# Kernel optimization log

Measured on AMD Instinct MI355X. Metric: run time of the kernel, lower is better.

The kernel has to match this reference:

```python
import jax, jax.numpy as jnp
import numpy as np

TEMP = 0.5
EPS = 1e-12  # matches torch F.normalize default eps


def _l2_normalize(x):
    n = jnp.sqrt(jnp.sum(x * x, axis=1, keepdims=True))
    return x / jnp.maximum(n, EPS)


def setup_inputs() -> dict:
    key = jax.random.key(0)
    k1, k2 = jax.random.split(key)
    B, D = 4096, 256
    return {
        "x_i": jax.random.normal(k1, (B, D), dtype=jnp.float32),
        "x_j": jax.random.normal(k2, (B, D), dtype=jnp.float32),
    }


def reference(x_i, x_j):
    B = x_i.shape[0]
    z = jnp.concatenate([_l2_normalize(x_i), _l2_normalize(x_j)], axis=0)  # [2B, D]
    # cosine similarity of normalized vectors == plain matmul
    sim = z @ z.T  # [2B, 2B]
    pos = jnp.concatenate([jnp.diagonal(sim, B), jnp.diagonal(sim, -B)], axis=0)  # [2B]
    neg_mask = 1.0 - jnp.eye(2 * B, dtype=sim.dtype)
    denom = jnp.sum(neg_mask * jnp.exp(sim / TEMP), axis=1)  # [2B]
    # -log(exp(pos/T) / denom) = -pos/T + log(denom)
    loss = jnp.sum(-(pos / TEMP) + jnp.log(denom)) / (2 * B)
    return loss
```

## Files before the change

### kernel.cpp

```cpp
#include <hip/hip_runtime.h>
#include <hip/hip_bf16.h>

#define B_ROWS 4096
#define NROWS  8192
#define D      256
#define TT     264
#define NBLK2  512
#define MAXT   9

typedef __attribute__((ext_vector_type(8))) short bf16x8;
typedef __attribute__((ext_vector_type(4))) float floatx4;

__global__ __launch_bounds__(256) void norm_pos_kernel(
    const float* __restrict__ xi, const float* __restrict__ xj,
    short* __restrict__ z, float* __restrict__ pos,
    float* __restrict__ selfdot, float* __restrict__ rowsum,
    float* __restrict__ out, unsigned int* __restrict__ counter) {
    int gt = blockIdx.x * 256 + threadIdx.x;
    if (gt < NROWS) rowsum[gt] = 0.f;
    if (gt == 0) { out[0] = 0.f; counter[0] = 0u; }

    int p    = blockIdx.x * 4 + (threadIdx.x >> 6);
    int lane = threadIdx.x & 63;
    float4 v1 = ((const float4*)(xi + (size_t)p * D))[lane];
    float4 v2 = ((const float4*)(xj + (size_t)p * D))[lane];
    float ss1 = v1.x * v1.x + v1.y * v1.y + v1.z * v1.z + v1.w * v1.w;
    float ss2 = v2.x * v2.x + v2.y * v2.y + v2.z * v2.z + v2.w * v2.w;
#pragma unroll
    for (int off = 32; off > 0; off >>= 1) {
        ss1 += __shfl_xor(ss1, off);
        ss2 += __shfl_xor(ss2, off);
    }
    float sc1 = 1.0f / fmaxf(sqrtf(ss1), 1e-12f);
    float sc2 = 1.0f / fmaxf(sqrtf(ss2), 1e-12f);

    union { __hip_bfloat16 h[4]; short4 s4; } u1, u2;
    u1.h[0] = __float2bfloat16(v1.x * sc1); u1.h[1] = __float2bfloat16(v1.y * sc1);
    u1.h[2] = __float2bfloat16(v1.z * sc1); u1.h[3] = __float2bfloat16(v1.w * sc1);
    u2.h[0] = __float2bfloat16(v2.x * sc2); u2.h[1] = __float2bfloat16(v2.y * sc2);
    u2.h[2] = __float2bfloat16(v2.z * sc2); u2.h[3] = __float2bfloat16(v2.w * sc2);
    ((short4*)(z + (size_t)p * D))[lane]            = u1.s4;
    ((short4*)(z + (size_t)(p + B_ROWS) * D))[lane] = u2.s4;

    float sd1 = 0.f, sd2 = 0.f, dp = 0.f;
#pragma unroll
    for (int j = 0; j < 4; j++) {
        float a = __bfloat162float(u1.h[j]);
        float b = __bfloat162float(u2.h[j]);
        sd1 += a * a; sd2 += b * b; dp += a * b;
    }
#pragma unroll
    for (int off = 32; off > 0; off >>= 1) {
        sd1 += __shfl_xor(sd1, off);
        sd2 += __shfl_xor(sd2, off);
        dp  += __shfl_xor(dp,  off);
    }
    if (lane == 0) {
        pos[p] = dp; pos[p + B_ROWS] = dp;
        selfdot[p] = sd1; selfdot[p + B_ROWS] = sd2;
    }
}

__global__ __launch_bounds__(256, 2) void sim_rowsum_kernel(
    const short* __restrict__ z, float* __restrict__ rowsum,
    const float* __restrict__ pos, const float* __restrict__ selfdot,
    unsigned int* __restrict__ counter, float* __restrict__ out) {
    __shared__ __align__(16) short Bbuf[2][8192];
    __shared__ float mirror_lds[MAXT][32];
    __shared__ unsigned int done_s;
    __shared__ float sdata[4];

    const int tid  = threadIdx.x;
    const int lane = tid & 63;
    const int w    = tid >> 6;
    const int lm   = lane & 15;
    const int lg   = lane >> 4;
    const int fxor = lm & 7;

    const int s   = blockIdx.x >> 5;
    const int q   = blockIdx.x & 31;
    const int L0  = 256 - 8 * s;
    const int cb  = (q * TT) >> 5;
    const int ce  = ((q + 1) * TT) >> 5;

    bf16x8 a[8][4];
    floatx4 acc[4][2];
    float rsacc[4][4];

#pragma unroll
    for (int mi = 0; mi < 4; mi++)
#pragma unroll
        for (int r = 0; r < 4; r++) rsacc[mi][r] = 0.f;

    auto decode = [&](int c, int& panel, int& colbase, bool& mirror) {
        int cloc;
        if (c < L0) { panel = s;      cloc = c; }
        else        { panel = 31 - s; cloc = c - L0; }
        colbase = panel * 256 + cloc * 32;
        mirror  = (cloc >= 8);
    };

    auto decodeCol = [&](int c) {
        int cloc, panel;
        if (c < L0) { panel = s;      cloc = c; }
        else        { panel = 31 - s; cloc = c - L0; }
        return panel * 256 + cloc * 32;
    };

    auto loadA = [&](int panel) {
#pragma unroll
        for (int kk = 0; kk < 8; kk++)
#pragma unroll
            for (int mi = 0; mi < 4; mi++)
                a[kk][mi] = *(const bf16x8*)(
                    z + (size_t)(panel * 256 + w * 64 + mi * 16 + lm) * D +
                    kk * 32 + lg * 8);
    };

    auto flushRs = [&](int panel) {
#pragma unroll
        for (int mi = 0; mi < 4; mi++)
#pragma unroll
            for (int r = 0; r < 4; r++) {
                float v = rsacc[mi][r];
                v += __shfl_xor(v, 1); v += __shfl_xor(v, 2);
                v += __shfl_xor(v, 4); v += __shfl_xor(v, 8);
                if (lm == 0)
                    atomicAdd(&rowsum[panel * 256 + w * 64 + mi * 16 + lg * 4 + r], v);
                rsacc[mi][r] = 0.f;
            }
    };

    auto stage = [&](int buf, int colbase) {
#pragma unroll
        for (int j = 0; j < 4; j++) {
            int col = w * 8 + j * 2 + (lane >> 5);
            int c16 = (lane & 31) ^ (col & 7);
            const short* src = z + (size_t)(colbase + col) * D + c16 * 8;
            __builtin_amdgcn_global_load_lds(
                (const __attribute__((address_space(1))) unsigned int*)src,
                (__attribute__((address_space(3))) unsigned int*)
                    &Bbuf[buf][(w * 4 + j) * 512],
                16, 0, 0);
        }
    };

    for (int e = tid; e < MAXT * 32; e += 256)
        ((float*)mirror_lds)[e] = 0.f;

    int panel, colbase; bool mirror;
    decode(cb, panel, colbase, mirror);
    int curpanel = panel;
    stage(0, colbase);
    loadA(panel);
    __syncthreads();

    for (int c = cb; c < ce; c++) {
        const int buf = (c - cb) & 1;
        decode(c, panel, colbase, mirror);

        if (c + 1 < ce)
            stage(buf ^ 1, decodeCol(c + 1));

        if (panel != curpanel) {
            flushRs(curpanel);
            loadA(panel);
            curpanel = panel;
        }

#pragma unroll
        for (int mi = 0; mi < 4; mi++)
#pragma unroll
            for (int ni = 0; ni < 2; ni++)
                acc[mi][ni] = (floatx4){0.f, 0.f, 0.f, 0.f};

#pragma unroll
        for (int kk = 0; kk < 8; kk++) {
            bf16x8 b0 = *(const bf16x8*)(
                &Bbuf[buf][((lm) * 32 + ((kk * 4 + lg) ^ fxor)) * 8]);
            bf16x8 b1 = *(const bf16x8*)(
                &Bbuf[buf][((16 + lm) * 32 + ((kk * 4 + lg) ^ fxor)) * 8]);
#pragma unroll
            for (int mi = 0; mi < 4; mi++)
                acc[mi][0] = __builtin_amdgcn_mfma_f32_16x16x32_bf16(
                    a[kk][mi], b0, acc[mi][0], 0, 0, 0);
#pragma unroll
            for (int mi = 0; mi < 4; mi++)
                acc[mi][1] = __builtin_amdgcn_mfma_f32_16x16x32_bf16(
                    a[kk][mi], b1, acc[mi][1], 0, 0, 0);
        }

        float cs0 = 0.f, cs1 = 0.f;
#pragma unroll
        for (int mi = 0; mi < 4; mi++)
#pragma unroll
            for (int r = 0; r < 4; r++) {
                float e0 = __expf(2.0f * acc[mi][0][r]);
                float e1 = __expf(2.0f * acc[mi][1][r]);
                rsacc[mi][r] += e0 + e1;
                cs0 += e0; cs1 += e1;
            }
        if (mirror) {
            cs0 += __shfl_xor(cs0, 16); cs0 += __shfl_xor(cs0, 32);
            cs1 += __shfl_xor(cs1, 16); cs1 += __shfl_xor(cs1, 32);
            if (lane < 16) {
                atomicAdd(&mirror_lds[c - cb][lane],      cs0);
                atomicAdd(&mirror_lds[c - cb][16 + lane], cs1);
            }
        }

        __syncthreads();
    }
    flushRs(curpanel);

    __syncthreads();
    {
        const int nt = ce - cb;
        for (int e = tid; e < nt * 32; e += 256) {
            int t = e >> 5, col = e & 31;
            int p2, cbase2; bool m2;
            decode(cb + t, p2, cbase2, m2);
            if (m2) atomicAdd(&rowsum[cbase2 + col], mirror_lds[t][col]);
        }
    }

    __syncthreads();
    if (tid == 0) {
        __threadfence();
        done_s = atomicAdd(counter, 1u);
    }
    __syncthreads();
    if (done_s == (unsigned int)(NBLK2 - 1)) {
        __threadfence();
        float acc_l = 0.f;
#pragma unroll 4
        for (int r = tid; r < NROWS; r += 256) {
            float rsv = __hip_atomic_load(&rowsum[r], __ATOMIC_RELAXED,
                                          __HIP_MEMORY_SCOPE_AGENT);
            float denom = rsv - __expf(2.0f * selfdot[r]);
            acc_l += -2.0f * pos[r] + logf(denom);
        }
#pragma unroll
        for (int off = 32; off > 0; off >>= 1) acc_l += __shfl_xor(acc_l, off);
        if (lane == 0) sdata[w] = acc_l;
        __syncthreads();
        if (tid == 0)
            out[0] = (sdata[0] + sdata[1] + sdata[2] + sdata[3]) / (float)NROWS;
    }
}

extern "C" void kernel_launch(void* const* d_in, const int* in_sizes, int n_in,
                              void* d_out, int out_size, void* d_ws, size_t ws_size,
                              hipStream_t stream) {
    const float* xi = (const float*)d_in[0];
    const float* xj = (const float*)d_in[1];
    float* out      = (float*)d_out;

    char* ws        = (char*)d_ws;
    short* z        = (short*)ws;
    float* rowsum   = (float*)(ws + (size_t)NROWS * D * 2);
    float* pos      = rowsum + NROWS;
    float* selfdot  = pos + NROWS;
    unsigned int* counter = (unsigned int*)(selfdot + NROWS);

    norm_pos_kernel<<<B_ROWS / 4, 256, 0, stream>>>(xi, xj, z, pos, selfdot,
                                                    rowsum, out, counter);
    sim_rowsum_kernel<<<NBLK2, 256, 0, stream>>>(z, rowsum, pos, selfdot,
                                                 counter, out);
}
```

Before: 103.7 us.

## Widen column tiles to 64 and push mirror sums straight to global atomics

Doubles the per-iteration column tile from 32 to 64 columns, so each wave computes a 64x64 block with 16 accumulators. This halves the number of tiles, block barriers and staging rounds per block, and each A-fragment load is reused across four B fragments. The LDS mirror-sum buffer and its final flush loop are removed. Mirror column sums now go directly to global rowsum with atomics from inside the loop. The change doubles the LDS staging buffer, raises register pressure from the larger accumulator array, and puts global atomics on the critical path of each iteration.

```diff
diff --git a/kernel.cpp b/kernel.cpp
--- a/kernel.cpp
+++ b/kernel.cpp
@@ -4,9 +4,8 @@
 #define B_ROWS 4096
 #define NROWS  8192
 #define D      256
-#define TT     264
+#define TT     132
 #define NBLK2  512
-#define MAXT   9
 
 typedef __attribute__((ext_vector_type(8))) short bf16x8;
 typedef __attribute__((ext_vector_type(4))) float floatx4;
@@ -65,8 +64,7 @@
     const short* __restrict__ z, float* __restrict__ rowsum,
     const float* __restrict__ pos, const float* __restrict__ selfdot,
     unsigned int* __restrict__ counter, float* __restrict__ out) {
-    __shared__ __align__(16) short Bbuf[2][8192];
-    __shared__ float mirror_lds[MAXT][32];
+    __shared__ __align__(16) short Bbuf[2][16384];
     __shared__ unsigned int done_s;
     __shared__ float sdata[4];
 
@@ -79,12 +77,12 @@
 
     const int s   = blockIdx.x >> 5;
     const int q   = blockIdx.x & 31;
-    const int L0  = 256 - 8 * s;
+    const int L0  = 128 - 4 * s;
     const int cb  = (q * TT) >> 5;
     const int ce  = ((q + 1) * TT) >> 5;
 
     bf16x8 a[8][4];
-    floatx4 acc[4][2];
+    floatx4 acc[4][4];
     float rsacc[4][4];
 
 #pragma unroll
@@ -96,15 +94,15 @@
         int cloc;
         if (c < L0) { panel = s;      cloc = c; }
         else        { panel = 31 - s; cloc = c - L0; }
-        colbase = panel * 256 + cloc * 32;
-        mirror  = (cloc >= 8);
+        colbase = panel * 256 + cloc * 64;
+        mirror  = (cloc >= 4);
     };
 
     auto decodeCol = [&](int c) {
         int cloc, panel;
         if (c < L0) { panel = s;      cloc = c; }
         else        { panel = 31 - s; cloc = c - L0; }
-        return panel * 256 + cloc * 32;
+        return panel * 256 + cloc * 64;
     };
 
     auto loadA = [&](int panel) {
@@ -133,20 +131,17 @@
 
     auto stage = [&](int buf, int colbase) {
 #pragma unroll
-        for (int j = 0; j < 4; j++) {
-            int col = w * 8 + j * 2 + (lane >> 5);
+        for (int j = 0; j < 8; j++) {
+            int col = w * 16 + j * 2 + (lane >> 5);
             int c16 = (lane & 31) ^ (col & 7);
             const short* src = z + (size_t)(colbase + col) * D + c16 * 8;
             __builtin_amdgcn_global_load_lds(
                 (const __attribute__((address_space(1))) unsigned int*)src,
                 (__attribute__((address_space(3))) unsigned int*)
-                    &Bbuf[buf][(w * 4 + j) * 512],
+                    &Bbuf[buf][(w * 8 + j) * 512],
                 16, 0, 0);
         }
     };
-
-    for (int e = tid; e < MAXT * 32; e += 256)
-        ((float*)mirror_lds)[e] = 0.f;
 
     int panel, colbase; bool mirror;
     decode(cb, panel, colbase, mirror);
@@ -171,58 +166,51 @@
 #pragma unroll
         for (int mi = 0; mi < 4; mi++)
 #pragma unroll
-            for (int ni = 0; ni < 2; ni++)
+            for (int ni = 0; ni < 4; ni++)
                 acc[mi][ni] = (floatx4){0.f, 0.f, 0.f, 0.f};
 
 #pragma unroll
         for (int kk = 0; kk < 8; kk++) {
-            bf16x8 b0 = *(const bf16x8*)(
-                &Bbuf[buf][((lm) * 32 + ((kk * 4 + lg) ^ fxor)) * 8]);
-            bf16x8 b1 = *(const bf16x8*)(
-                &Bbuf[buf][((16 + lm) * 32 + ((kk * 4 + lg) ^ fxor)) * 8]);
-#pragma unroll
-            for (int mi = 0; mi < 4; mi++)
-                acc[mi][0] = __builtin_amdgcn_mfma_f32_16x16x32_bf16(
-                    a[kk][mi], b0, acc[mi][0], 0, 0, 0);
-#pragma unroll
-            for (int mi = 0; mi < 4; mi++)
-                acc[mi][1] = __builtin_amdgcn_mfma_f32_16x16x32_bf16(
-                    a[kk][mi], b1, acc[mi][1], 0, 0, 0);
-        }
-
-        float cs0 = 0.f, cs1 = 0.f;
+            bf16x8 b[4];
+#pragma unroll
+            for (int ni = 0; ni < 4; ni++)
+                b[ni] = *(const bf16x8*)(
+                    &Bbuf[buf][((ni * 16 + lm) * 32 + ((kk * 4 + lg) ^ fxor)) * 8]);
+#pragma unroll
+            for (int ni = 0; ni < 4; ni++)
+#pragma unroll
+                for (int mi = 0; mi < 4; mi++)
+                    acc[mi][ni] = __builtin_amdgcn_mfma_f32_16x16x32_bf16(
+                        a[kk][mi], b[ni], acc[mi][ni], 0, 0, 0);
+        }
+
+        float cs[4] = {0.f, 0.f, 0.f, 0.f};
 #pragma unroll
         for (int mi = 0; mi < 4; mi++)
 #pragma unroll
-            for (int r = 0; r < 4; r++) {
-                float e0 = __expf(2.0f * acc[mi][0][r]);
-                float e1 = __expf(2.0f * acc[mi][1][r]);
-                rsacc[mi][r] += e0 + e1;
-                cs0 += e0; cs1 += e1;
+            for (int ni = 0; ni < 4; ni++)
+#pragma unroll
+                for (int r = 0; r < 4; r++) {
+                    float e = __expf(2.0f * acc[mi][ni][r]);
+                    rsacc[mi][r] += e;
+                    cs[ni] += e;
+                }
+        if (mirror) {
+#pragma unroll
+            for (int ni = 0; ni < 4; ni++) {
+                cs[ni] += __shfl_xor(cs[ni], 16);
+                cs[ni] += __shfl_xor(cs[ni], 32);
             }
-        if (mirror) {
-            cs0 += __shfl_xor(cs0, 16); cs0 += __shfl_xor(cs0, 32);
-            cs1 += __shfl_xor(cs1, 16); cs1 += __shfl_xor(cs1, 32);
             if (lane < 16) {
-                atomicAdd(&mirror_lds[c - cb][lane],      cs0);
-                atomicAdd(&mirror_lds[c - cb][16 + lane], cs1);
+#pragma unroll
+                for (int ni = 0; ni < 4; ni++)
+                    atomicAdd(&rowsum[colbase + ni * 16 + lane], cs[ni]);
             }
         }
 
         __syncthreads();
     }
     flushRs(curpanel);
-
-    __syncthreads();
-    {
-        const int nt = ce - cb;
-        for (int e = tid; e < nt * 32; e += 256) {
-            int t = e >> 5, col = e & 31;
-            int p2, cbase2; bool m2;
-            decode(cb + t, p2, cbase2, m2);
-            if (m2) atomicAdd(&rowsum[cbase2 + col], mirror_lds[t][col]);
-        }
-    }
 
     __syncthreads();
     if (tid == 0) {
```

After: 107.8 us. +3.9%, slower.
